# Performance work log

Hardware: AMD Instinct MI355X
Metric: run time of the kernel (lower is better)

Reference implementation:

```python
import jax, jax.numpy as jnp
import numpy as np

N = 4096        # n_nodes
IN = 512        # in_features
HEADS = 8       # n_heads
HID = 64        # n_hidden = out_features // n_heads
SLOPE = 0.2     # leaky relu negative slope


def setup_inputs() -> dict:
    key = jax.random.key(0)
    k1, k2, k3, k4 = jax.random.split(key, 4)
    h = jax.random.normal(k1, (N, IN), dtype=jnp.float32)
    W = jax.random.normal(k2, (IN, HEADS * HID), dtype=jnp.float32) * 0.05
    a = jax.random.normal(k3, (2 * HID,), dtype=jnp.float32) * 0.05
    adj = jax.random.uniform(k4, (N, N)) < 0.01
    adj = adj | jnp.eye(N, dtype=bool)
    return {"h": h, "adj_mat": adj[..., None], "W": W, "a": a}


def reference(h, adj_mat, W, a):
    # g[i, h, f] = per-head projected features
    g = (h @ W).reshape(N, HEADS, HID)
    # attention Linear on concat([g_i, g_j]) splits into two dot products
    a_l, a_r = a[:HID], a[HID:]
    el = jnp.einsum('ihf,f->ih', g, a_l)   # score contribution of target i
    er = jnp.einsum('jhf,f->jh', g, a_r)   # score contribution of source j
    e = el[:, None, :] + er[None, :, :]    # [N, N, HEADS]
    e = jnp.where(e >= 0, e, SLOPE * e)    # LeakyReLU
    e = jnp.where(adj_mat, e, -jnp.inf)    # mask non-edges (adj broadcasts over heads)
    attn = jax.nn.softmax(e, axis=1)       # softmax over source nodes j
    out = jnp.einsum('ijh,jhf->ihf', attn, g)
    return out.reshape(N, HEADS * HID)     # is_concat=True
```

## Files before the change

### kernel.cpp

```cpp
#include <hip/hip_runtime.h>
#include <cstdint>
#include <cstddef>

#define N_NODES 4096
#define IN_DIM  512
#define HEADS   8
#define HID     64
#define OUTF    (HEADS * HID)
#define SLOPE   0.2f
#define MAXD    256
#define MAXD2   128

typedef __bf16 bf16_t;
typedef __attribute__((ext_vector_type(8))) __bf16 bf16x8;
typedef __attribute__((ext_vector_type(4))) float    f32x4;

#define GLD16(gp, lp)                                                                  \
    __builtin_amdgcn_global_load_lds((const __attribute__((address_space(1))) void*)(gp), \
                                     (__attribute__((address_space(3))) void*)(lp), 16, 0, 0)

__device__ __forceinline__ unsigned short to_bf16_u(float x) {
    uint32_t u = __builtin_bit_cast(uint32_t, x);
    u += 0x7fffu + ((u >> 16) & 1u);
    return (unsigned short)(u >> 16);
}
__device__ __forceinline__ float bfbits_to_f(unsigned short b) {
    uint32_t u = ((uint32_t)b) << 16;
    return __builtin_bit_cast(float, u);
}

__global__ __launch_bounds__(256) void streampack(const int* __restrict__ adj,
                                                  unsigned short* __restrict__ bm16,
                                                  const float* __restrict__ W,
                                                  unsigned short* __restrict__ whiT,
                                                  unsigned short* __restrict__ wloT) {
    const int b = blockIdx.x;
    const int tid = threadIdx.x;
    if (b < 4096) {
        const int t = b * 256 + tid;
        const int4* src = (const int4*)adj + (size_t)t * 4;
        const int4 v0 = src[0], v1 = src[1], v2 = src[2], v3 = src[3];
        uint32_t m = 0;
        m |= (v0.x != 0) ? 1u << 0 : 0;  m |= (v0.y != 0) ? 1u << 1 : 0;
        m |= (v0.z != 0) ? 1u << 2 : 0;  m |= (v0.w != 0) ? 1u << 3 : 0;
        m |= (v1.x != 0) ? 1u << 4 : 0;  m |= (v1.y != 0) ? 1u << 5 : 0;
        m |= (v1.z != 0) ? 1u << 6 : 0;  m |= (v1.w != 0) ? 1u << 7 : 0;
        m |= (v2.x != 0) ? 1u << 8 : 0;  m |= (v2.y != 0) ? 1u << 9 : 0;
        m |= (v2.z != 0) ? 1u << 10 : 0; m |= (v2.w != 0) ? 1u << 11 : 0;
        m |= (v3.x != 0) ? 1u << 12 : 0; m |= (v3.y != 0) ? 1u << 13 : 0;
        m |= (v3.z != 0) ? 1u << 14 : 0; m |= (v3.w != 0) ? 1u << 15 : 0;
        bm16[t] = (unsigned short)m;
    } else {
        const int idx = (b - 4096) * 256 + tid;
        const int c   = idx & 511;
        const int kq  = (idx >> 9) * 4;
        ushort4 hv, lv;
        float w0 = W[(size_t)(kq + 0) * OUTF + c];
        float w1 = W[(size_t)(kq + 1) * OUTF + c];
        float w2 = W[(size_t)(kq + 2) * OUTF + c];
        float w3 = W[(size_t)(kq + 3) * OUTF + c];
        hv.x = to_bf16_u(w0); lv.x = to_bf16_u(w0 - bfbits_to_f(hv.x));
        hv.y = to_bf16_u(w1); lv.y = to_bf16_u(w1 - bfbits_to_f(hv.y));
        hv.z = to_bf16_u(w2); lv.z = to_bf16_u(w2 - bfbits_to_f(hv.z));
        hv.w = to_bf16_u(w3); lv.w = to_bf16_u(w3 - bfbits_to_f(hv.w));
        *(ushort4*)&whiT[(size_t)c * IN_DIM + kq] = hv;
        *(ushort4*)&wloT[(size_t)c * IN_DIM + kq] = lv;
    }
}

__global__ __launch_bounds__(256) void gemm_f32A(const float* __restrict__ Hf,
                                                 const bf16_t* __restrict__ BhiT,
                                                 const bf16_t* __restrict__ BloT,
                                                 const float* __restrict__ a,
                                                 unsigned short* __restrict__ Gb,
                                                 float* __restrict__ el,
                                                 float* __restrict__ er) {
    __shared__ float  As[2][64 * 64];
    __shared__ bf16_t Bh[2][64 * 64];
    __shared__ bf16_t Bl[2][64 * 64];
    __shared__ float  elp[2][64], erp[2][64];

    const int tid = threadIdx.x;
    const int wid = tid >> 6;
    const int lane = tid & 63;
    const int head = blockIdx.x >> 6;
    const int i0 = (blockIdx.x & 63) * 64;
    const int j0 = head * 64;
    const int l15 = lane & 15, kq = lane >> 4;

    size_t aoff[4];
#pragma unroll
    for (int c4 = 0; c4 < 4; ++c4) {
        const int row = wid * 16 + c4 * 4 + (lane >> 4);
        const int sc = (lane & 15) ^ (row & 15);
        aoff[c4] = (size_t)(i0 + row) * IN_DIM + sc * 4;
    }
    const int sr0 = wid * 16 + (lane >> 3);
    const int scb = (lane & 7) ^ (sr0 & 7);
    const size_t boff = (size_t)(j0 + sr0) * IN_DIM + scb * 8;

    const int wm = wid >> 1, wn = wid & 1;
    int aro[2][2][2], bro[2][2];
#pragma unroll
    for (int m = 0; m < 2; ++m) {
        const int row = wm * 32 + m * 16 + l15;
#pragma unroll
        for (int ks = 0; ks < 2; ++ks) {
            const int c0 = ks * 8 + kq * 2;
            aro[m][ks][0] = row * 64 + ((c0 + 0) ^ (row & 15)) * 4;
            aro[m][ks][1] = row * 64 + ((c0 + 1) ^ (row & 15)) * 4;
        }
    }
#pragma unroll
    for (int n = 0; n < 2; ++n) {
        const int col = wn * 32 + n * 16 + l15;
#pragma unroll
        for (int ks = 0; ks < 2; ++ks)
            bro[n][ks] = col * 64 + (((ks * 4 + kq) ^ (col & 7)) * 8);
    }

    f32x4 acc[2][2] = {};

    auto stage = [&](int buf, int t) {
        const size_t k0 = (size_t)t * 64;
#pragma unroll
        for (int c4 = 0; c4 < 4; ++c4)
            GLD16(Hf + aoff[c4] + k0, &As[buf][(wid * 16 + c4 * 4) * 64]);
        GLD16(BhiT + boff + k0,                      &Bh[buf][(wid * 16) * 64]);
        GLD16(BhiT + boff + (size_t)8 * IN_DIM + k0, &Bh[buf][(wid * 16 + 8) * 64]);
        GLD16(BloT + boff + k0,                      &Bl[buf][(wid * 16) * 64]);
        GLD16(BloT + boff + (size_t)8 * IN_DIM + k0, &Bl[buf][(wid * 16 + 8) * 64]);
    };

    stage(0, 0);
    for (int t = 0; t < 8; ++t) {
        const int cur = t & 1;
        if (t < 7) {
            stage(cur ^ 1, t + 1);
            asm volatile("s_waitcnt vmcnt(8)" ::: "memory");
        } else {
            asm volatile("s_waitcnt vmcnt(0)" ::: "memory");
        }
        __builtin_amdgcn_s_barrier();
        asm volatile("" ::: "memory");

        bf16x8 af[2][2];
#pragma unroll
        for (int m = 0; m < 2; ++m)
#pragma unroll
            for (int ks = 0; ks < 2; ++ks) {
                const f32x4 lo4 = *(const f32x4*)&As[cur][aro[m][ks][0]];
                const f32x4 hi4 = *(const f32x4*)&As[cur][aro[m][ks][1]];
                bf16x8 v;
                v[0] = (bf16_t)lo4[0]; v[1] = (bf16_t)lo4[1];
                v[2] = (bf16_t)lo4[2]; v[3] = (bf16_t)lo4[3];
                v[4] = (bf16_t)hi4[0]; v[5] = (bf16_t)hi4[1];
                v[6] = (bf16_t)hi4[2]; v[7] = (bf16_t)hi4[3];
                af[m][ks] = v;
            }
        bf16x8 bh2[2][2], bl2[2][2];
#pragma unroll
        for (int n = 0; n < 2; ++n)
#pragma unroll
            for (int ks = 0; ks < 2; ++ks) {
                bh2[n][ks] = *(const bf16x8*)&Bh[cur][bro[n][ks]];
                bl2[n][ks] = *(const bf16x8*)&Bl[cur][bro[n][ks]];
            }
#pragma unroll
        for (int ks = 0; ks < 2; ++ks)
#pragma unroll
            for (int m = 0; m < 2; ++m)
#pragma unroll
                for (int n = 0; n < 2; ++n) {
                    acc[m][n] = __builtin_amdgcn_mfma_f32_16x16x32_bf16(af[m][ks], bh2[n][ks], acc[m][n], 0, 0, 0);
                    acc[m][n] = __builtin_amdgcn_mfma_f32_16x16x32_bf16(af[m][ks], bl2[n][ks], acc[m][n], 0, 0, 0);
                }

        __builtin_amdgcn_s_barrier();
        asm volatile("" ::: "memory");
    }

#pragma unroll
    for (int m = 0; m < 2; ++m)
#pragma unroll
        for (int n = 0; n < 2; ++n) {
            const int col = j0 + wn * 32 + n * 16 + l15;
#pragma unroll
            for (int q = 0; q < 4; ++q) {
                const int row = i0 + wm * 32 + m * 16 + kq * 4 + q;
                Gb[(size_t)row * OUTF + col] = to_bf16_u(acc[m][n][q]);
            }
        }

    float al[2], arr[2];
#pragma unroll
    for (int n = 0; n < 2; ++n) {
        al[n]  = a[wn * 32 + n * 16 + l15];
        arr[n] = a[64 + wn * 32 + n * 16 + l15];
    }
#pragma unroll
    for (int m = 0; m < 2; ++m)
#pragma unroll
        for (int q = 0; q < 4; ++q) {
            float pe = 0.f, pr = 0.f;
#pragma unroll
            for (int n = 0; n < 2; ++n) {
                const float v = acc[m][n][q];
                pe = fmaf(v, al[n], pe);
                pr = fmaf(v, arr[n], pr);
            }
#pragma unroll
            for (int off = 1; off < 16; off <<= 1) {
                pe += __shfl_xor(pe, off);
                pr += __shfl_xor(pr, off);
            }
            if (l15 == 0) {
                const int lrow = wm * 32 + m * 16 + kq * 4 + q;
                elp[wn][lrow] = pe;
                erp[wn][lrow] = pr;
            }
        }
    __syncthreads();
    if (tid < 64) {
        el[(size_t)(i0 + tid) * HEADS + head] = elp[0][tid] + elp[1][tid];
        er[(size_t)(i0 + tid) * HEADS + head] = erp[0][tid] + erp[1][tid];
    }
}

__global__ __launch_bounds__(512) void gat_attn_wave(const unsigned long long* __restrict__ bm64,
                                                     const unsigned short* __restrict__ Gb,
                                                     const float* __restrict__ el,
                                                     const float* __restrict__ er,
                                                     float* __restrict__ out) {
    __shared__ int   nbr[4][2][MAXD2];
    __shared__ float pw[4][8][MAXD2 + 8];
    __shared__ float red[4][2][OUTF];
    __shared__ float sinv[4][8];
    const int tid = threadIdx.x;
    const int lane = tid & 63;
    const int wid = tid >> 6;
    const int r = wid >> 1, sub = wid & 1;
    const int i = blockIdx.x * 4 + r;

    unsigned long long q = bm64[(size_t)i * 64 + lane];
    const int c = __popcll(q);
    int inc = c;
#pragma unroll
    for (int off = 1; off < 64; off <<= 1) {
        const int t = __shfl_up(inc, off);
        if (lane >= off) inc += t;
    }
    const int deg = min(__shfl(inc, 63), MAXD2);
    int pos = inc - c;
    while (q) {
        const int b = __builtin_ctzll(q);
        q &= q - 1;
        if (pos < MAXD2) nbr[r][sub][pos] = lane * 64 + b;
        ++pos;
    }
    asm volatile("s_waitcnt lgkmcnt(0)" ::: "memory");
    __builtin_amdgcn_wave_barrier();

    const float4 el4 = *(const float4*)(el + (size_t)i * 8 + sub * 4);
    float mx[4] = {-1e30f, -1e30f, -1e30f, -1e30f};
    for (int j = lane; j < deg; j += 64) {
        const int nj = nbr[r][sub][j];
        const float4 er4 = *(const float4*)(er + (size_t)nj * 8 + sub * 4);
        float e[4] = {el4.x + er4.x, el4.y + er4.y, el4.z + er4.z, el4.w + er4.w};
#pragma unroll
        for (int hh = 0; hh < 4; ++hh) {
            e[hh] = (e[hh] >= 0.f) ? e[hh] : SLOPE * e[hh];
            pw[r][sub * 4 + hh][j] = e[hh];
            mx[hh] = fmaxf(mx[hh], e[hh]);
        }
    }
#pragma unroll
    for (int off = 1; off < 64; off <<= 1)
#pragma unroll
        for (int hh = 0; hh < 4; ++hh) mx[hh] = fmaxf(mx[hh], __shfl_xor(mx[hh], off));

    float s4[4] = {};
    for (int j = lane; j < deg; j += 64) {
#pragma unroll
        for (int hh = 0; hh < 4; ++hh) {
            const float pe = __expf(pw[r][sub * 4 + hh][j] - mx[hh]);
            pw[r][sub * 4 + hh][j] = pe;
            s4[hh] += pe;
        }
    }
#pragma unroll
    for (int off = 1; off < 64; off <<= 1)
#pragma unroll
        for (int hh = 0; hh < 4; ++hh) s4[hh] += __shfl_xor(s4[hh], off);
    if (lane == 0) {
#pragma unroll
        for (int hh = 0; hh < 4; ++hh) sinv[r][sub * 4 + hh] = 1.f / s4[hh];
    }
    __syncthreads();

    const int myhead = lane >> 3;
    float a8[8] = {};
    const unsigned short* gl = Gb + lane * 8;
#pragma unroll 4
    for (int j = sub; j < deg; j += 2) {
        const int nj = nbr[r][sub][j];
        const float w = pw[r][myhead][j];
        const uint4 v = *(const uint4*)(gl + (size_t)nj * OUTF);
        a8[0] = fmaf(w, bfbits_to_f((unsigned short)(v.x & 0xffffu)), a8[0]);
        a8[1] = fmaf(w, bfbits_to_f((unsigned short)(v.x >> 16)),     a8[1]);
        a8[2] = fmaf(w, bfbits_to_f((unsigned short)(v.y & 0xffffu)), a8[2]);
        a8[3] = fmaf(w, bfbits_to_f((unsigned short)(v.y >> 16)),     a8[3]);
        a8[4] = fmaf(w, bfbits_to_f((unsigned short)(v.z & 0xffffu)), a8[4]);
        a8[5] = fmaf(w, bfbits_to_f((unsigned short)(v.z >> 16)),     a8[5]);
        a8[6] = fmaf(w, bfbits_to_f((unsigned short)(v.w & 0xffffu)), a8[6]);
        a8[7] = fmaf(w, bfbits_to_f((unsigned short)(v.w >> 16)),     a8[7]);
    }
    float4 lo = {a8[0], a8[1], a8[2], a8[3]};
    float4 hi = {a8[4], a8[5], a8[6], a8[7]};
    *(float4*)&red[r][sub][lane * 8 + 0] = lo;
    *(float4*)&red[r][sub][lane * 8 + 4] = hi;
    __syncthreads();

#pragma unroll
    for (int rr = 0; rr < 4; ++rr) {
        const float v = red[rr][0][tid] + red[rr][1][tid];
        out[(size_t)(blockIdx.x * 4 + rr) * OUTF + tid] = v * sinv[rr][tid >> 6];
    }
}

__global__ __launch_bounds__(256) void gemm_f32(const float* __restrict__ A,
                                                const float* __restrict__ B,
                                                float* __restrict__ C) {
    __shared__ float As[16][68];
    __shared__ float Bs[16][64];
    const int tid = threadIdx.x;
    const int tx = tid & 15, ty = tid >> 4;
    const int i0 = blockIdx.y * 64;
    const int j0 = blockIdx.x * 64;
    const int ar = tid >> 2;
    const int ac = (tid & 3) << 2;
    const int bk = tid >> 4;
    const int bc = (tid & 15) << 2;
    float acc[4][4] = {};
    for (int k0 = 0; k0 < IN_DIM; k0 += 16) {
        const float4 av = *(const float4*)(A + (size_t)(i0 + ar) * IN_DIM + k0 + ac);
        const float4 bv = *(const float4*)(B + (size_t)(k0 + bk) * OUTF + j0 + bc);
        __syncthreads();
        As[ac + 0][ar] = av.x; As[ac + 1][ar] = av.y;
        As[ac + 2][ar] = av.z; As[ac + 3][ar] = av.w;
        *(float4*)&Bs[bk][bc] = bv;
        __syncthreads();
#pragma unroll
        for (int k = 0; k < 16; ++k) {
            const float4 a4 = *(const float4*)&As[k][ty << 2];
            const float4 b4 = *(const float4*)&Bs[k][tx << 2];
            const float am[4] = {a4.x, a4.y, a4.z, a4.w};
            const float bn[4] = {b4.x, b4.y, b4.z, b4.w};
#pragma unroll
            for (int m = 0; m < 4; ++m)
#pragma unroll
                for (int n = 0; n < 4; ++n)
                    acc[m][n] = fmaf(am[m], bn[n], acc[m][n]);
        }
    }
#pragma unroll
    for (int m = 0; m < 4; ++m) {
        float4 v = {acc[m][0], acc[m][1], acc[m][2], acc[m][3]};
        *(float4*)(C + (size_t)(i0 + (ty << 2) + m) * OUTF + j0 + (tx << 2)) = v;
    }
}

__global__ __launch_bounds__(512) void el_er_kernel(const float* __restrict__ g,
                                                    const float* __restrict__ a,
                                                    float* __restrict__ el,
                                                    float* __restrict__ er) {
    const int i = blockIdx.x;
    const int wid = threadIdx.x >> 6;
    const int lane = threadIdx.x & 63;
    const float v = g[(size_t)i * OUTF + wid * HID + lane];
    float pl = v * a[lane];
    float pr = v * a[HID + lane];
#pragma unroll
    for (int off = 1; off < 64; off <<= 1) {
        pl += __shfl_xor(pl, off);
        pr += __shfl_xor(pr, off);
    }
    if (lane == 0) {
        el[(size_t)i * HEADS + wid] = pl;
        er[(size_t)i * HEADS + wid] = pr;
    }
}

__global__ __launch_bounds__(512) void gat_attn_f32(const int* __restrict__ adj,
                                                    const float* __restrict__ g,
                                                    const float* __restrict__ el,
                                                    const float* __restrict__ er,
                                                    float* __restrict__ out) {
    const int i = blockIdx.x;
    const int tid = threadIdx.x;
    const int lane = tid & 63;
    const int wid = tid >> 6;

    __shared__ int   nbr[MAXD];
    __shared__ float p[HEADS][MAXD + 2];
    __shared__ float red[8][256];
    __shared__ float sinv[8];
    __shared__ int   wave_base[8];
    __shared__ int   s_deg;

    const int4* row = (const int4*)(adj + (size_t)i * N_NODES);
    const int4 w0 = row[tid * 2 + 0];
    const int4 w1 = row[tid * 2 + 1];
    uint32_t msk = 0;
    if (w0.x) msk |= 1u;   if (w0.y) msk |= 2u;
    if (w0.z) msk |= 4u;   if (w0.w) msk |= 8u;
    if (w1.x) msk |= 16u;  if (w1.y) msk |= 32u;
    if (w1.z) msk |= 64u;  if (w1.w) msk |= 128u;

    const int c = __popc(msk);
    int inc = c;
#pragma unroll
    for (int off = 1; off < 64; off <<= 1) {
        const int t = __shfl_up(inc, off);
        if (lane >= off) inc += t;
    }
    if (lane == 63) wave_base[wid] = inc;
    __syncthreads();
    if (tid == 0) {
        int run = 0;
#pragma unroll
        for (int w = 0; w < 8; ++w) { const int t = wave_base[w]; wave_base[w] = run; run += t; }
        s_deg = run;
    }
    __syncthreads();
    int pos = wave_base[wid] + inc - c;
#pragma unroll
    for (int b = 0; b < 8; ++b) {
        if (msk & (1u << b)) {
            if (pos < MAXD) nbr[pos] = tid * 8 + b;
            ++pos;
        }
    }
    __syncthreads();
    const int deg = min(s_deg, MAXD);

    const float eli = el[(size_t)i * HEADS + wid];
    float m = -1e30f;
    for (int j = lane; j < deg; j += 64) {
        float e = eli + er[(size_t)nbr[j] * HEADS + wid];
        e = (e >= 0.f) ? e : SLOPE * e;
        p[wid][j] = e;
        m = fmaxf(m, e);
    }
#pragma unroll
    for (int off = 1; off < 64; off <<= 1) m = fmaxf(m, __shfl_xor(m, off));
    float s = 0.f;
    for (int j = lane; j < deg; j += 64) {
        const float pe = __expf(p[wid][j] - m);
        p[wid][j] = pe;
        s += pe;
    }
#pragma unroll
    for (int off = 1; off < 64; off <<= 1) s += __shfl_xor(s, off);
    if (lane == 0) sinv[wid] = 1.f / s;
    __syncthreads();

    const int half = wid >> 2, jslot = wid & 3;
    const int head = half * 4 + (lane >> 4);
    const int f4 = (lane & 15) * 4;
    const float* gbase = g + (size_t)head * HID + f4;
    float4 acc = {0.f, 0.f, 0.f, 0.f};
#pragma unroll 4
    for (int j = jslot; j < deg; j += 4) {
        const int nj = nbr[j];
        const float w = p[head][j];
        const float4 v = *(const float4*)(gbase + (size_t)nj * OUTF);
        acc.x = fmaf(w, v.x, acc.x);
        acc.y = fmaf(w, v.y, acc.y);
        acc.z = fmaf(w, v.z, acc.z);
        acc.w = fmaf(w, v.w, acc.w);
    }
    *(float4*)&red[wid][(lane >> 4) * 64 + f4] = acc;
    __syncthreads();

    const int hf = tid >> 8, loc = tid & 255;
    const float v = red[hf * 4 + 0][loc] + red[hf * 4 + 1][loc] +
                    red[hf * 4 + 2][loc] + red[hf * 4 + 3][loc];
    out[(size_t)i * OUTF + tid] = v * sinv[tid >> 6];
}

extern "C" void kernel_launch(void* const* d_in, const int* in_sizes, int n_in,
                              void* d_out, int out_size, void* d_ws, size_t ws_size,
                              hipStream_t stream) {
    const float* h   = (const float*)d_in[0];
    const int*   adj = (const int*)d_in[1];
    const float* W   = (const float*)d_in[2];
    const float* a   = (const float*)d_in[3];
    float* out = (float*)d_out;
    char* ws = (char*)d_ws;

    const size_t G_OFF  = 0;
    const size_t EL_OFF = 8388608;
    const size_t ER_OFF = 8519680;
    const size_t BM_OFF = 8650752;
    const size_t WHI_OFF = 10747904;
    const size_t WLO_OFF = 11272192;
    const size_t NEED_FULL = 11796480;

    float* el = (float*)(ws + EL_OFF);
    float* er = (float*)(ws + ER_OFF);

    if (ws_size >= NEED_FULL) {
        unsigned short* gbf  = (unsigned short*)(ws + G_OFF);
        unsigned short* bm   = (unsigned short*)(ws + BM_OFF);
        unsigned short* whiT = (unsigned short*)(ws + WHI_OFF);
        unsigned short* wloT = (unsigned short*)(ws + WLO_OFF);
        streampack<<<4352, 256, 0, stream>>>(adj, bm, W, whiT, wloT);
        gemm_f32A<<<512, 256, 0, stream>>>(h, (const bf16_t*)whiT, (const bf16_t*)wloT,
                                           a, gbf, el, er);
        gat_attn_wave<<<1024, 512, 0, stream>>>((const unsigned long long*)bm, gbf, el, er, out);
    } else {
        float* g = (float*)(ws + G_OFF);
        gemm_f32<<<dim3(8, 64), 256, 0, stream>>>(h, W, g);
        el_er_kernel<<<N_NODES, 512, 0, stream>>>(g, a, el, er);
        gat_attn_f32<<<N_NODES, 512, 0, stream>>>(adj, g, el, er, out);
    }
}
```

Baseline: 42.90 us.

## Fuse adjacency bitmask packing into attention kernel, split row halves per wave

Drops the separate adjacency-to-bitmask pass and has each attention wave read its half of the int adjacency row directly, building the neighbour list in place. Each of the two waves per row now covers all 8 heads over half the columns, and the two halves are merged through shared-memory max and sum values. This removes one full pass over the 64 MB adjacency plus the bitmask write and read. The cost is a wider per-wave register footprint, an extra block barrier, and a per-half neighbour cap of 80, which could truncate rows with more neighbours in one half.

```diff
diff --git a/kernel.cpp b/kernel.cpp
--- a/kernel.cpp
+++ b/kernel.cpp
@@ -9,7 +9,7 @@
 #define OUTF    (HEADS * HID)
 #define SLOPE   0.2f
 #define MAXD    256
-#define MAXD2   128
+#define MAXDH   80
 
 typedef __bf16 bf16_t;
 typedef __attribute__((ext_vector_type(8))) __bf16 bf16x8;
@@ -29,43 +29,23 @@
     return __builtin_bit_cast(float, u);
 }
 
-__global__ __launch_bounds__(256) void streampack(const int* __restrict__ adj,
-                                                  unsigned short* __restrict__ bm16,
-                                                  const float* __restrict__ W,
-                                                  unsigned short* __restrict__ whiT,
-                                                  unsigned short* __restrict__ wloT) {
-    const int b = blockIdx.x;
-    const int tid = threadIdx.x;
-    if (b < 4096) {
-        const int t = b * 256 + tid;
-        const int4* src = (const int4*)adj + (size_t)t * 4;
-        const int4 v0 = src[0], v1 = src[1], v2 = src[2], v3 = src[3];
-        uint32_t m = 0;
-        m |= (v0.x != 0) ? 1u << 0 : 0;  m |= (v0.y != 0) ? 1u << 1 : 0;
-        m |= (v0.z != 0) ? 1u << 2 : 0;  m |= (v0.w != 0) ? 1u << 3 : 0;
-        m |= (v1.x != 0) ? 1u << 4 : 0;  m |= (v1.y != 0) ? 1u << 5 : 0;
-        m |= (v1.z != 0) ? 1u << 6 : 0;  m |= (v1.w != 0) ? 1u << 7 : 0;
-        m |= (v2.x != 0) ? 1u << 8 : 0;  m |= (v2.y != 0) ? 1u << 9 : 0;
-        m |= (v2.z != 0) ? 1u << 10 : 0; m |= (v2.w != 0) ? 1u << 11 : 0;
-        m |= (v3.x != 0) ? 1u << 12 : 0; m |= (v3.y != 0) ? 1u << 13 : 0;
-        m |= (v3.z != 0) ? 1u << 14 : 0; m |= (v3.w != 0) ? 1u << 15 : 0;
-        bm16[t] = (unsigned short)m;
-    } else {
-        const int idx = (b - 4096) * 256 + tid;
-        const int c   = idx & 511;
-        const int kq  = (idx >> 9) * 4;
-        ushort4 hv, lv;
-        float w0 = W[(size_t)(kq + 0) * OUTF + c];
-        float w1 = W[(size_t)(kq + 1) * OUTF + c];
-        float w2 = W[(size_t)(kq + 2) * OUTF + c];
-        float w3 = W[(size_t)(kq + 3) * OUTF + c];
-        hv.x = to_bf16_u(w0); lv.x = to_bf16_u(w0 - bfbits_to_f(hv.x));
-        hv.y = to_bf16_u(w1); lv.y = to_bf16_u(w1 - bfbits_to_f(hv.y));
-        hv.z = to_bf16_u(w2); lv.z = to_bf16_u(w2 - bfbits_to_f(hv.z));
-        hv.w = to_bf16_u(w3); lv.w = to_bf16_u(w3 - bfbits_to_f(hv.w));
-        *(ushort4*)&whiT[(size_t)c * IN_DIM + kq] = hv;
-        *(ushort4*)&wloT[(size_t)c * IN_DIM + kq] = lv;
-    }
+__global__ __launch_bounds__(256) void wprep(const float* __restrict__ W,
+                                             unsigned short* __restrict__ whiT,
+                                             unsigned short* __restrict__ wloT) {
+    const int idx = blockIdx.x * 256 + threadIdx.x;
+    const int c   = idx & 511;
+    const int kq  = (idx >> 9) * 4;
+    ushort4 hv, lv;
+    float w0 = W[(size_t)(kq + 0) * OUTF + c];
+    float w1 = W[(size_t)(kq + 1) * OUTF + c];
+    float w2 = W[(size_t)(kq + 2) * OUTF + c];
+    float w3 = W[(size_t)(kq + 3) * OUTF + c];
+    hv.x = to_bf16_u(w0); lv.x = to_bf16_u(w0 - bfbits_to_f(hv.x));
+    hv.y = to_bf16_u(w1); lv.y = to_bf16_u(w1 - bfbits_to_f(hv.y));
+    hv.z = to_bf16_u(w2); lv.z = to_bf16_u(w2 - bfbits_to_f(hv.z));
+    hv.w = to_bf16_u(w3); lv.w = to_bf16_u(w3 - bfbits_to_f(hv.w));
+    *(ushort4*)&whiT[(size_t)c * IN_DIM + kq] = hv;
+    *(ushort4*)&wloT[(size_t)c * IN_DIM + kq] = lv;
 }
 
 __global__ __launch_bounds__(256) void gemm_f32A(const float* __restrict__ Hf,
@@ -227,74 +207,96 @@
     }
 }
 
-__global__ __launch_bounds__(512) void gat_attn_wave(const unsigned long long* __restrict__ bm64,
-                                                     const unsigned short* __restrict__ Gb,
-                                                     const float* __restrict__ el,
-                                                     const float* __restrict__ er,
-                                                     float* __restrict__ out) {
-    __shared__ int   nbr[4][2][MAXD2];
-    __shared__ float pw[4][8][MAXD2 + 8];
+__global__ __launch_bounds__(512) void gat_attn_fused(const int* __restrict__ adj,
+                                                      const unsigned short* __restrict__ Gb,
+                                                      const float* __restrict__ el,
+                                                      const float* __restrict__ er,
+                                                      float* __restrict__ out) {
+    __shared__ int   nbr[4][2][MAXDH];
+    __shared__ float pw[4][2][8][MAXDH];
     __shared__ float red[4][2][OUTF];
-    __shared__ float sinv[4][8];
+    __shared__ float rmax[4][2][8];
+    __shared__ float rsum[4][2][8];
+
     const int tid = threadIdx.x;
     const int lane = tid & 63;
     const int wid = tid >> 6;
     const int r = wid >> 1, sub = wid & 1;
     const int i = blockIdx.x * 4 + r;
 
-    unsigned long long q = bm64[(size_t)i * 64 + lane];
-    const int c = __popcll(q);
-    int inc = c;
+    const int4* arow = (const int4*)(adj + (size_t)i * N_NODES + sub * 2048);
+    uint32_t mask = 0;
+#pragma unroll
+    for (int c = 0; c < 8; ++c) {
+        const int4 v = arow[c * 64 + lane];
+        if (v.x) mask |= 1u << (c * 4 + 0);
+        if (v.y) mask |= 1u << (c * 4 + 1);
+        if (v.z) mask |= 1u << (c * 4 + 2);
+        if (v.w) mask |= 1u << (c * 4 + 3);
+    }
+    const int cnt = __popc(mask);
+    int inc = cnt;
 #pragma unroll
     for (int off = 1; off < 64; off <<= 1) {
         const int t = __shfl_up(inc, off);
         if (lane >= off) inc += t;
     }
-    const int deg = min(__shfl(inc, 63), MAXD2);
-    int pos = inc - c;
-    while (q) {
-        const int b = __builtin_ctzll(q);
-        q &= q - 1;
-        if (pos < MAXD2) nbr[r][sub][pos] = lane * 64 + b;
+    const int degh = min(__shfl(inc, 63), MAXDH);
+    int pos = inc - cnt;
+    while (mask) {
+        const int b = __builtin_ctzll((unsigned long long)mask);
+        mask &= mask - 1;
+        if (pos < MAXDH) nbr[r][sub][pos] = sub * 2048 + ((b >> 2) * 64 + lane) * 4 + (b & 3);
         ++pos;
     }
-    asm volatile("s_waitcnt lgkmcnt(0)" ::: "memory");
-    __builtin_amdgcn_wave_barrier();
-
-    const float4 el4 = *(const float4*)(el + (size_t)i * 8 + sub * 4);
-    float mx[4] = {-1e30f, -1e30f, -1e30f, -1e30f};
-    for (int j = lane; j < deg; j += 64) {
+
+    const float4 el_lo = *(const float4*)(el + (size_t)i * 8);
+    const float4 el_hi = *(const float4*)(el + (size_t)i * 8 + 4);
+    float mx[8];
+#pragma unroll
+    for (int h = 0; h < 8; ++h) mx[h] = -1e30f;
+    for (int j = lane; j < degh; j += 64) {
         const int nj = nbr[r][sub][j];
-        const float4 er4 = *(const float4*)(er + (size_t)nj * 8 + sub * 4);
-        float e[4] = {el4.x + er4.x, el4.y + er4.y, el4.z + er4.z, el4.w + er4.w};
-#pragma unroll
-        for (int hh = 0; hh < 4; ++hh) {
-            e[hh] = (e[hh] >= 0.f) ? e[hh] : SLOPE * e[hh];
-            pw[r][sub * 4 + hh][j] = e[hh];
-            mx[hh] = fmaxf(mx[hh], e[hh]);
+        const float4 er_lo = *(const float4*)(er + (size_t)nj * 8);
+        const float4 er_hi = *(const float4*)(er + (size_t)nj * 8 + 4);
+        float e[8] = {el_lo.x + er_lo.x, el_lo.y + er_lo.y, el_lo.z + er_lo.z, el_lo.w + er_lo.w,
+                      el_hi.x + er_hi.x, el_hi.y + er_hi.y, el_hi.z + er_hi.z, el_hi.w + er_hi.w};
+#pragma unroll
+        for (int h = 0; h < 8; ++h) {
+            e[h] = (e[h] >= 0.f) ? e[h] : SLOPE * e[h];
+            pw[r][sub][h][j] = e[h];
+            mx[h] = fmaxf(mx[h], e[h]);
         }
     }
 #pragma unroll
     for (int off = 1; off < 64; off <<= 1)
 #pragma unroll
-        for (int hh = 0; hh < 4; ++hh) mx[hh] = fmaxf(mx[hh], __shfl_xor(mx[hh], off));
-
-    float s4[4] = {};
-    for (int j = lane; j < deg; j += 64) {
-#pragma unroll
-        for (int hh = 0; hh < 4; ++hh) {
-            const float pe = __expf(pw[r][sub * 4 + hh][j] - mx[hh]);
-            pw[r][sub * 4 + hh][j] = pe;
-            s4[hh] += pe;
+        for (int h = 0; h < 8; ++h) mx[h] = fmaxf(mx[h], __shfl_xor(mx[h], off));
+    if (lane == 0) {
+#pragma unroll
+        for (int h = 0; h < 8; ++h) rmax[r][sub][h] = mx[h];
+    }
+    __syncthreads();
+
+    float m8[8];
+#pragma unroll
+    for (int h = 0; h < 8; ++h) m8[h] = fmaxf(rmax[r][0][h], rmax[r][1][h]);
+    float s8[8] = {};
+    for (int j = lane; j < degh; j += 64) {
+#pragma unroll
+        for (int h = 0; h < 8; ++h) {
+            const float pe = __expf(pw[r][sub][h][j] - m8[h]);
+            pw[r][sub][h][j] = pe;
+            s8[h] += pe;
         }
     }
 #pragma unroll
     for (int off = 1; off < 64; off <<= 1)
 #pragma unroll
-        for (int hh = 0; hh < 4; ++hh) s4[hh] += __shfl_xor(s4[hh], off);
+        for (int h = 0; h < 8; ++h) s8[h] += __shfl_xor(s8[h], off);
     if (lane == 0) {
 #pragma unroll
-        for (int hh = 0; hh < 4; ++hh) sinv[r][sub * 4 + hh] = 1.f / s4[hh];
+        for (int h = 0; h < 8; ++h) rsum[r][sub][h] = s8[h];
     }
     __syncthreads();
 
@@ -302,9 +304,9 @@
     float a8[8] = {};
     const unsigned short* gl = Gb + lane * 8;
 #pragma unroll 4
-    for (int j = sub; j < deg; j += 2) {
+    for (int j = 0; j < degh; ++j) {
         const int nj = nbr[r][sub][j];
-        const float w = pw[r][myhead][j];
+        const float w = pw[r][sub][myhead][j];
         const uint4 v = *(const uint4*)(gl + (size_t)nj * OUTF);
         a8[0] = fmaf(w, bfbits_to_f((unsigned short)(v.x & 0xffffu)), a8[0]);
         a8[1] = fmaf(w, bfbits_to_f((unsigned short)(v.x >> 16)),     a8[1]);
@@ -323,8 +325,10 @@
 
 #pragma unroll
     for (int rr = 0; rr < 4; ++rr) {
+        const int hh = tid >> 6;
+        const float s = rsum[rr][0][hh] + rsum[rr][1][hh];
         const float v = red[rr][0][tid] + red[rr][1][tid];
-        out[(size_t)(blockIdx.x * 4 + rr) * OUTF + tid] = v * sinv[rr][tid >> 6];
+        out[(size_t)(blockIdx.x * 4 + rr) * OUTF + tid] = v / s;
     }
 }
 
@@ -502,23 +506,21 @@
     const size_t G_OFF  = 0;
     const size_t EL_OFF = 8388608;
     const size_t ER_OFF = 8519680;
-    const size_t BM_OFF = 8650752;
-    const size_t WHI_OFF = 10747904;
-    const size_t WLO_OFF = 11272192;
-    const size_t NEED_FULL = 11796480;
+    const size_t WHI_OFF = 8650752;
+    const size_t WLO_OFF = 9175040;
+    const size_t NEED_FULL = 9699328;
 
     float* el = (float*)(ws + EL_OFF);
     float* er = (float*)(ws + ER_OFF);
 
     if (ws_size >= NEED_FULL) {
         unsigned short* gbf  = (unsigned short*)(ws + G_OFF);
-        unsigned short* bm   = (unsigned short*)(ws + BM_OFF);
         unsigned short* whiT = (unsigned short*)(ws + WHI_OFF);
         unsigned short* wloT = (unsigned short*)(ws + WLO_OFF);
-        streampack<<<4352, 256, 0, stream>>>(adj, bm, W, whiT, wloT);
+        wprep<<<256, 256, 0, stream>>>(W, whiT, wloT);
         gemm_f32A<<<512, 256, 0, stream>>>(h, (const bf16_t*)whiT, (const bf16_t*)wloT,
                                            a, gbf, el, er);
-        gat_attn_wave<<<1024, 512, 0, stream>>>((const unsigned long long*)bm, gbf, el, er, out);
+        gat_attn_fused<<<1024, 512, 0, stream>>>(adj, gbf, el, er, out);
     } else {
         float* g = (float*)(ws + G_OFF);
         gemm_f32<<<dim3(8, 64), 256, 0, stream>>>(h, W, g);
```

Result: slower. 48.23 us (+12.4%).

## Interleave adjacency bitmask packing into the projection GEMM kernel launch

Applied to the files above, without the earlier changes.

The adjacency-packing blocks move out of the prep kernel and into the GEMM launch, interleaved 8 pack blocks per GEMM block, so memory-bound packing overlaps with MFMA-bound projection work. The W split into bf16 hi/lo runs as its own small kernel before that launch. This hides the roughly 64MB adjacency read behind the GEMM compute. In exchange, GEMM blocks now share the GPU with many lightweight pack blocks, which could change scheduling, and LDS is allocated for every block, which may limit how many pack blocks are resident at once.

```diff
diff --git a/kernel.cpp b/kernel.cpp
--- a/kernel.cpp
+++ b/kernel.cpp
@@ -29,62 +29,70 @@
     return __builtin_bit_cast(float, u);
 }
 
-__global__ __launch_bounds__(256) void streampack(const int* __restrict__ adj,
-                                                  unsigned short* __restrict__ bm16,
-                                                  const float* __restrict__ W,
-                                                  unsigned short* __restrict__ whiT,
-                                                  unsigned short* __restrict__ wloT) {
-    const int b = blockIdx.x;
-    const int tid = threadIdx.x;
-    if (b < 4096) {
-        const int t = b * 256 + tid;
-        const int4* src = (const int4*)adj + (size_t)t * 4;
-        const int4 v0 = src[0], v1 = src[1], v2 = src[2], v3 = src[3];
-        uint32_t m = 0;
-        m |= (v0.x != 0) ? 1u << 0 : 0;  m |= (v0.y != 0) ? 1u << 1 : 0;
-        m |= (v0.z != 0) ? 1u << 2 : 0;  m |= (v0.w != 0) ? 1u << 3 : 0;
-        m |= (v1.x != 0) ? 1u << 4 : 0;  m |= (v1.y != 0) ? 1u << 5 : 0;
-        m |= (v1.z != 0) ? 1u << 6 : 0;  m |= (v1.w != 0) ? 1u << 7 : 0;
-        m |= (v2.x != 0) ? 1u << 8 : 0;  m |= (v2.y != 0) ? 1u << 9 : 0;
-        m |= (v2.z != 0) ? 1u << 10 : 0; m |= (v2.w != 0) ? 1u << 11 : 0;
-        m |= (v3.x != 0) ? 1u << 12 : 0; m |= (v3.y != 0) ? 1u << 13 : 0;
-        m |= (v3.z != 0) ? 1u << 14 : 0; m |= (v3.w != 0) ? 1u << 15 : 0;
-        bm16[t] = (unsigned short)m;
-    } else {
-        const int idx = (b - 4096) * 256 + tid;
-        const int c   = idx & 511;
-        const int kq  = (idx >> 9) * 4;
-        ushort4 hv, lv;
-        float w0 = W[(size_t)(kq + 0) * OUTF + c];
-        float w1 = W[(size_t)(kq + 1) * OUTF + c];
-        float w2 = W[(size_t)(kq + 2) * OUTF + c];
-        float w3 = W[(size_t)(kq + 3) * OUTF + c];
-        hv.x = to_bf16_u(w0); lv.x = to_bf16_u(w0 - bfbits_to_f(hv.x));
-        hv.y = to_bf16_u(w1); lv.y = to_bf16_u(w1 - bfbits_to_f(hv.y));
-        hv.z = to_bf16_u(w2); lv.z = to_bf16_u(w2 - bfbits_to_f(hv.z));
-        hv.w = to_bf16_u(w3); lv.w = to_bf16_u(w3 - bfbits_to_f(hv.w));
-        *(ushort4*)&whiT[(size_t)c * IN_DIM + kq] = hv;
-        *(ushort4*)&wloT[(size_t)c * IN_DIM + kq] = lv;
-    }
-}
-
-__global__ __launch_bounds__(256) void gemm_f32A(const float* __restrict__ Hf,
-                                                 const bf16_t* __restrict__ BhiT,
-                                                 const bf16_t* __restrict__ BloT,
-                                                 const float* __restrict__ a,
-                                                 unsigned short* __restrict__ Gb,
-                                                 float* __restrict__ el,
-                                                 float* __restrict__ er) {
+__device__ __forceinline__ void pack_item(int u, const int* __restrict__ adj,
+                                          unsigned short* __restrict__ bm16) {
+    const int4* src = (const int4*)adj + (size_t)u * 4;
+    const int4 v0 = src[0], v1 = src[1], v2 = src[2], v3 = src[3];
+    uint32_t m = 0;
+    m |= (v0.x != 0) ? 1u << 0 : 0;  m |= (v0.y != 0) ? 1u << 1 : 0;
+    m |= (v0.z != 0) ? 1u << 2 : 0;  m |= (v0.w != 0) ? 1u << 3 : 0;
+    m |= (v1.x != 0) ? 1u << 4 : 0;  m |= (v1.y != 0) ? 1u << 5 : 0;
+    m |= (v1.z != 0) ? 1u << 6 : 0;  m |= (v1.w != 0) ? 1u << 7 : 0;
+    m |= (v2.x != 0) ? 1u << 8 : 0;  m |= (v2.y != 0) ? 1u << 9 : 0;
+    m |= (v2.z != 0) ? 1u << 10 : 0; m |= (v2.w != 0) ? 1u << 11 : 0;
+    m |= (v3.x != 0) ? 1u << 12 : 0; m |= (v3.y != 0) ? 1u << 13 : 0;
+    m |= (v3.z != 0) ? 1u << 14 : 0; m |= (v3.w != 0) ? 1u << 15 : 0;
+    bm16[u] = (unsigned short)m;
+}
+
+__global__ __launch_bounds__(256) void wprep(const float* __restrict__ W,
+                                             unsigned short* __restrict__ whiT,
+                                             unsigned short* __restrict__ wloT) {
+    const int idx = blockIdx.x * 256 + threadIdx.x;
+    const int c   = idx & 511;
+    const int kq  = (idx >> 9) * 4;
+    ushort4 hv, lv;
+    float w0 = W[(size_t)(kq + 0) * OUTF + c];
+    float w1 = W[(size_t)(kq + 1) * OUTF + c];
+    float w2 = W[(size_t)(kq + 2) * OUTF + c];
+    float w3 = W[(size_t)(kq + 3) * OUTF + c];
+    hv.x = to_bf16_u(w0); lv.x = to_bf16_u(w0 - bfbits_to_f(hv.x));
+    hv.y = to_bf16_u(w1); lv.y = to_bf16_u(w1 - bfbits_to_f(hv.y));
+    hv.z = to_bf16_u(w2); lv.z = to_bf16_u(w2 - bfbits_to_f(hv.z));
+    hv.w = to_bf16_u(w3); lv.w = to_bf16_u(w3 - bfbits_to_f(hv.w));
+    *(ushort4*)&whiT[(size_t)c * IN_DIM + kq] = hv;
+    *(ushort4*)&wloT[(size_t)c * IN_DIM + kq] = lv;
+}
+
+__global__ __launch_bounds__(256) void fused_gp(const float* __restrict__ Hf,
+                                                const bf16_t* __restrict__ BhiT,
+                                                const bf16_t* __restrict__ BloT,
+                                                const float* __restrict__ a,
+                                                unsigned short* __restrict__ Gb,
+                                                float* __restrict__ el,
+                                                float* __restrict__ er,
+                                                const int* __restrict__ adj,
+                                                unsigned short* __restrict__ bm16) {
     __shared__ float  As[2][64 * 64];
     __shared__ bf16_t Bh[2][64 * 64];
     __shared__ bf16_t Bl[2][64 * 64];
     __shared__ float  elp[2][64], erp[2][64];
 
+    const int bid = blockIdx.x;
     const int tid = threadIdx.x;
+    const int q9 = bid / 9;
+
+    if (bid - q9 * 9 != 0) {
+        const int pid = bid - 1 - q9;
+        pack_item(pid * 256 + tid, adj, bm16);
+        return;
+    }
+
+    const int gid = q9;
     const int wid = tid >> 6;
     const int lane = tid & 63;
-    const int head = blockIdx.x >> 6;
-    const int i0 = (blockIdx.x & 63) * 64;
+    const int head = gid >> 6;
+    const int i0 = (gid & 63) * 64;
     const int j0 = head * 64;
     const int l15 = lane & 15, kq = lane >> 4;
 
@@ -120,7 +128,6 @@
     }
 
     f32x4 acc[2][2] = {};
-
     auto stage = [&](int buf, int t) {
         const size_t k0 = (size_t)t * 64;
 #pragma unroll
@@ -175,7 +182,6 @@
                     acc[m][n] = __builtin_amdgcn_mfma_f32_16x16x32_bf16(af[m][ks], bh2[n][ks], acc[m][n], 0, 0, 0);
                     acc[m][n] = __builtin_amdgcn_mfma_f32_16x16x32_bf16(af[m][ks], bl2[n][ks], acc[m][n], 0, 0, 0);
                 }
-
         __builtin_amdgcn_s_barrier();
         asm volatile("" ::: "memory");
     }
@@ -205,9 +211,8 @@
             float pe = 0.f, pr = 0.f;
 #pragma unroll
             for (int n = 0; n < 2; ++n) {
-                const float v = acc[m][n][q];
-                pe = fmaf(v, al[n], pe);
-                pr = fmaf(v, arr[n], pr);
+                pe = fmaf(acc[m][n][q], al[n], pe);
+                pr = fmaf(acc[m][n][q], arr[n], pr);
             }
 #pragma unroll
             for (int off = 1; off < 16; off <<= 1) {
@@ -499,10 +504,10 @@
     float* out = (float*)d_out;
     char* ws = (char*)d_ws;
 
-    const size_t G_OFF  = 0;
-    const size_t EL_OFF = 8388608;
-    const size_t ER_OFF = 8519680;
-    const size_t BM_OFF = 8650752;
+    const size_t G_OFF   = 0;
+    const size_t EL_OFF  = 8388608;
+    const size_t ER_OFF  = 8519680;
+    const size_t BM_OFF  = 8650752;
     const size_t WHI_OFF = 10747904;
     const size_t WLO_OFF = 11272192;
     const size_t NEED_FULL = 11796480;
@@ -511,13 +516,13 @@
     float* er = (float*)(ws + ER_OFF);
 
     if (ws_size >= NEED_FULL) {
-        unsigned short* gbf  = (unsigned short*)(ws + G_OFF);
-        unsigned short* bm   = (unsigned short*)(ws + BM_OFF);
-        unsigned short* whiT = (unsigned short*)(ws + WHI_OFF);
-        unsigned short* wloT = (unsigned short*)(ws + WLO_OFF);
-        streampack<<<4352, 256, 0, stream>>>(adj, bm, W, whiT, wloT);
-        gemm_f32A<<<512, 256, 0, stream>>>(h, (const bf16_t*)whiT, (const bf16_t*)wloT,
-                                           a, gbf, el, er);
+        unsigned short*     gbf  = (unsigned short*)(ws + G_OFF);
+        unsigned short*     bm   = (unsigned short*)(ws + BM_OFF);
+        unsigned short*     whiT = (unsigned short*)(ws + WHI_OFF);
+        unsigned short*     wloT = (unsigned short*)(ws + WLO_OFF);
+        wprep<<<256, 256, 0, stream>>>(W, whiT, wloT);
+        fused_gp<<<4608, 256, 0, stream>>>(h, (const bf16_t*)whiT, (const bf16_t*)wloT,
+                                           a, gbf, el, er, adj, bm);
         gat_attn_wave<<<1024, 512, 0, stream>>>((const unsigned long long*)bm, gbf, el, er, out);
     } else {
         float* g = (float*)(ws + G_OFF);
```

New measurement: 51.02 us. 18.9% more time.
